# Performance work log

Hardware: AMD Instinct MI355X
Metric: run time of the kernel (lower is better)

## Reference

```python
import jax, jax.numpy as jnp
import numpy as np

T, B, E, H = 2048, 2, 1024, 16
D = E // H

def setup_inputs() -> dict:
    key = jax.random.key(0)
    ks = jax.random.split(key, 5)
    s = 1.0 / np.sqrt(E)  # keep projection weights at sane scale
    return {
        "query": jax.random.normal(ks[0], (T, B, E), jnp.float32),
        "Wq": jax.random.normal(ks[1], (E, E), jnp.float32) * s,
        "bq": jnp.zeros((E,), jnp.float32),
        "Wk": jax.random.normal(ks[2], (E, E), jnp.float32) * s,
        "bk": jnp.zeros((E,), jnp.float32),
        "Wv": jax.random.normal(ks[3], (E, E), jnp.float32) * s,
        "bv": jnp.zeros((E,), jnp.float32),
        "Wo": jax.random.normal(ks[4], (E, E), jnp.float32) * s,
        "bo": jnp.zeros((E,), jnp.float32),
    }

def reference(query, Wq, bq, Wk, bk, Wv, bv, Wo, bo):
    # query: [T, B, E] (fairseq time-first). self-attention path.
    scaling = D ** -0.5
    q = (query @ Wq.T + bq) * scaling          # [T,B,E]
    k = query @ Wk.T + bk                      # [T,B,E]
    v = query @ Wv.T + bv                      # [T,B,E]
    # split heads: [T,B,H,D]
    q = q.reshape(T, B, H, D)
    k = k.reshape(T, B, H, D)
    v = v.reshape(T, B, H, D)
    # attention scores [B,H,T,S]
    scores = jnp.einsum("tbhd,sbhd->bhts", q, k)
    probs = jax.nn.softmax(scores, axis=-1)
    # weighted values -> [T,B,H,D]
    attn = jnp.einsum("bhts,sbhd->tbhd", probs, v).reshape(T, B, E)
    return attn @ Wo.T + bo                    # [T,B,E]
```

## Files before the change

kernel.cpp:

```cpp
#include <hip/hip_runtime.h>
#include <hip/hip_bf16.h>

#define T_DIM 2048

typedef __attribute__((ext_vector_type(8))) short short8_t;
typedef short8_t __attribute__((may_alias)) short8_a;
typedef __attribute__((ext_vector_type(4))) short short4_t;
typedef short4_t __attribute__((may_alias)) short4_a;
typedef __attribute__((ext_vector_type(4))) float f32x4;
typedef __attribute__((ext_vector_type(16))) float f32x16;
typedef __attribute__((ext_vector_type(4))) float float4_t;
typedef float4_t __attribute__((may_alias)) float4_a;
typedef __attribute__((ext_vector_type(4))) unsigned int u32x4;

__device__ __forceinline__ short f2bf(float f) {
    unsigned int u = __builtin_bit_cast(unsigned int, f);
    unsigned int r = (u + 0x7fffu + ((u >> 16) & 1u)) >> 16;
    return (short)r;
}

__device__ __forceinline__ void gl_lds16(const short* g, short* l) {
    __builtin_amdgcn_global_load_lds(
        (const __attribute__((address_space(1))) void*)g,
        (__attribute__((address_space(3))) void*)l, 16, 0, 0);
}

__global__ __launch_bounds__(256) void cvt_kernel(const float* __restrict__ in,
                                                  short* __restrict__ out, int n) {
    int i = (blockIdx.x * 256 + threadIdx.x) * 8;
    if (i >= n) return;
    float4_a a = *(const float4_a*)(in + i);
    float4_a b = *(const float4_a*)(in + i + 4);
    short8_a r;
    r[0] = f2bf(a[0]); r[1] = f2bf(a[1]); r[2] = f2bf(a[2]); r[3] = f2bf(a[3]);
    r[4] = f2bf(b[0]); r[5] = f2bf(b[1]); r[6] = f2bf(b[2]); r[7] = f2bf(b[3]);
    *(short8_a*)(out + i) = r;
}

__global__ __launch_bounds__(256) void cvt_w4(const float* __restrict__ w0, const float* __restrict__ w1,
                                              const float* __restrict__ w2, const float* __restrict__ w3,
                                              short* __restrict__ o0, short* __restrict__ o1,
                                              short* __restrict__ o2, short* __restrict__ o3) {
    const float* in; short* out;
    switch (blockIdx.y) {
        case 0: in = w0; out = o0; break;
        case 1: in = w1; out = o1; break;
        case 2: in = w2; out = o2; break;
        default: in = w3; out = o3; break;
    }
    int i = (blockIdx.x * 256 + threadIdx.x) * 8;
    float4_a a = *(const float4_a*)(in + i);
    float4_a b = *(const float4_a*)(in + i + 4);
    short8_a r;
    r[0] = f2bf(a[0]); r[1] = f2bf(a[1]); r[2] = f2bf(a[2]); r[3] = f2bf(a[3]);
    r[4] = f2bf(b[0]); r[5] = f2bf(b[1]); r[6] = f2bf(b[2]); r[7] = f2bf(b[3]);
    *(short8_a*)(out + i) = r;
}

template <int BM, int BN, int MODE>
__global__ __launch_bounds__(256) void gemm_lds(const short* __restrict__ A,
                                                const short* __restrict__ W,
                                                const float* __restrict__ b0,
                                                const float* __restrict__ b1,
                                                const float* __restrict__ b2,
                                                short* __restrict__ o0,
                                                short* __restrict__ o1,
                                                short* __restrict__ o2,
                                                float* __restrict__ of) {
    constexpr int FM = BM / 32;
    constexpr int FN = BN / 32;
    __shared__ short As[BM * 32];
    __shared__ short Bs[BN * 32];

    const int tid = threadIdx.x;
    const int l = tid & 63, w = tid >> 6;
    const int wm = w >> 1, wn = w & 1;
    const int m0 = blockIdx.y * BM, n0 = blockIdx.x * BN;
    const int l15 = l & 15, l4 = l >> 4;
    const int lr = l >> 2, lc = (l & 3) * 8;

    f32x4 acc[FM][FN];
#pragma unroll
    for (int i = 0; i < FM; i++)
#pragma unroll
        for (int j = 0; j < FN; j++) {
            f32x4 z = {0.f, 0.f, 0.f, 0.f};
            acc[i][j] = z;
        }

    const short* Ab = A + (m0 + lr) * 1024 + lc;
    const short* Wb = W + (n0 + lr) * 1024 + lc;

    for (int k0 = 0; k0 < 1024; k0 += 32) {
#pragma unroll
        for (int j = 0; j < BM / 64; j++) {
            int base = (j * 4 + w) * 16;
            gl_lds16(Ab + base * 1024 + k0, &As[base * 32]);
        }
#pragma unroll
        for (int j = 0; j < BN / 64; j++) {
            int base = (j * 4 + w) * 16;
            gl_lds16(Wb + base * 1024 + k0, &Bs[base * 32]);
        }
        __syncthreads();

        short8_t af[FM], bf[FN];
#pragma unroll
        for (int m = 0; m < FM; m++)
            af[m] = *(const short8_a*)&As[(wm * (BM / 2) + m * 16 + l15) * 32 + l4 * 8];
#pragma unroll
        for (int n = 0; n < FN; n++)
            bf[n] = *(const short8_a*)&Bs[(wn * (BN / 2) + n * 16 + l15) * 32 + l4 * 8];
#pragma unroll
        for (int m = 0; m < FM; m++)
#pragma unroll
            for (int n = 0; n < FN; n++)
                acc[m][n] = __builtin_amdgcn_mfma_f32_16x16x32_bf16(af[m], bf[n], acc[m][n], 0, 0, 0);
        __syncthreads();
    }

    if (MODE == 3) {
#pragma unroll
        for (int n = 0; n < FN; n++) {
            int col = n0 + wn * (BN / 2) + n * 16 + l15;
            float bv = b0[col];
#pragma unroll
            for (int m = 0; m < FM; m++)
#pragma unroll
                for (int i = 0; i < 4; i++) {
                    int row = m0 + wm * (BM / 2) + m * 16 + l4 * 4 + i;
                    of[row * 1024 + col] = acc[m][n][i] + bv;
                }
        }
    } else {
        const int proj = n0 >> 10;
        const float* bias = proj == 0 ? b0 : (proj == 1 ? b1 : b2);
        short* outp = proj == 0 ? o0 : (proj == 1 ? o1 : o2);
#pragma unroll
        for (int n = 0; n < FN; n++) {
            int cw = (n0 + wn * (BN / 2) + n * 16 + l15) & 1023;
            float bv = bias[cw];
            int h = cw >> 6, d = cw & 63;
#pragma unroll
            for (int m = 0; m < FM; m++)
#pragma unroll
                for (int i = 0; i < 4; i++) {
                    int row = m0 + wm * (BM / 2) + m * 16 + l4 * 4 + i;
                    float v = acc[m][n][i] + bv;
                    if (proj == 0) v *= 0.18033688011112042f;
                    int bb = row & 1, t = row >> 1;
                    if (proj == 2)
                        outp[((bb * 16 + h) * 64 + d) * 2048 + t] = f2bf(v);
                    else
                        outp[((bb * 16 + h) * 2048 + t) * 64 + d] = f2bf(v);
                }
        }
    }
}

__device__ __forceinline__ float max16(const f32x16 v) {
    float a0 = fmaxf(fmaxf(v[0], v[1]), v[2]);
    float a1 = fmaxf(fmaxf(v[3], v[4]), v[5]);
    float a2 = fmaxf(fmaxf(v[6], v[7]), v[8]);
    float a3 = fmaxf(fmaxf(v[9], v[10]), v[11]);
    float a4 = fmaxf(fmaxf(v[12], v[13]), v[14]);
    float b0 = fmaxf(fmaxf(a0, a1), v[15]);
    float b1 = fmaxf(fmaxf(a2, a3), a4);
    return fmaxf(b0, b1);
}

__global__ __launch_bounds__(256) void flash_attn(const short* __restrict__ Q,
                                                  const short* __restrict__ K,
                                                  const short* __restrict__ Vt,
                                                  short* __restrict__ O) {
    __shared__ short Ks[2][64 * 64];
    __shared__ short Vs[2][64 * 64];

    const int tid = threadIdx.x, l = tid & 63, w = tid >> 6;
    const int l31 = l & 31, hi = l >> 5;
    const int e = l31 & 7;
    const int bh = blockIdx.y;
    const int b = bh >> 4, hh = bh & 15;
    const int qrow = blockIdx.x * 128 + w * 32 + l31;

    const short* Qp = Q + bh * (T_DIM * 64);
    const short* Kp = K + bh * (T_DIM * 64);
    const short* Vp = Vt + bh * (64 * T_DIM);

    short8_t qf[4];
#pragma unroll
    for (int c = 0; c < 4; c++)
        qf[c] = *(const short8_a*)&Qp[qrow * 64 + c * 16 + hi * 8];

    f32x16 oacc[2];
    f32x16 lacc;
#pragma unroll
    for (int i = 0; i < 16; i++) { oacc[0][i] = 0.f; oacc[1][i] = 0.f; lacc[i] = 0.f; }
    float mrow = -1e30f;

    short8_t ones;
#pragma unroll
    for (int j = 0; j < 8; j++) ones[j] = (short)0x3F80;

    const int srow0 = tid >> 3, sch = tid & 7;
    const int srow1 = srow0 + 32;
    const int kslot0 = (sch ^ (srow0 & 7)) * 8;
    const int kslot1 = (sch ^ (srow1 & 7)) * 8;

    short8_t kpre[2], vpre[2];
    kpre[0] = *(const short8_a*)&Kp[srow0 * 64 + sch * 8];
    kpre[1] = *(const short8_a*)&Kp[srow1 * 64 + sch * 8];
    vpre[0] = *(const short8_a*)&Vp[srow0 * 2048 + sch * 8];
    vpre[1] = *(const short8_a*)&Vp[srow1 * 2048 + sch * 8];
    *(short8_a*)&Ks[0][srow0 * 64 + kslot0] = kpre[0];
    *(short8_a*)&Ks[0][srow1 * 64 + kslot1] = kpre[1];
    *(short8_a*)&Vs[0][srow0 * 64 + kslot0] = vpre[0];
    *(short8_a*)&Vs[0][srow1 * 64 + kslot1] = vpre[1];

    auto body = [&](const short* kc, const short* vc, short* kn, short* vn, int it) {
        __syncthreads();
        if (it + 1 < 32) {
            int s0 = (it + 1) * 64;
            kpre[0] = *(const short8_a*)&Kp[(s0 + srow0) * 64 + sch * 8];
            kpre[1] = *(const short8_a*)&Kp[(s0 + srow1) * 64 + sch * 8];
            vpre[0] = *(const short8_a*)&Vp[srow0 * 2048 + s0 + sch * 8];
            vpre[1] = *(const short8_a*)&Vp[srow1 * 2048 + s0 + sch * 8];
        }

        f32x16 st[2];
#pragma unroll
        for (int r = 0; r < 2; r++) {
#pragma unroll
            for (int i = 0; i < 16; i++) st[r][i] = 0.f;
#pragma unroll
            for (int c = 0; c < 4; c++) {
                short8_t kf = *(const short8_a*)&kc[(r * 32 + l31) * 64 + ((2 * c + hi) ^ e) * 8];
                st[r] = __builtin_amdgcn_mfma_f32_32x32x16_bf16(kf, qf[c], st[r], 0, 0, 0);
            }
        }

        float pmax = fmaxf(max16(st[0]), max16(st[1]));
        pmax = fmaxf(pmax, __shfl_xor(pmax, 32));
        if (__any(pmax > mrow + 8.f)) {
            float mn = fmaxf(mrow, pmax);
            float sc = exp2f(mrow - mn);
            mrow = mn;
            lacc[0] *= sc;
#pragma unroll
            for (int dd = 0; dd < 2; dd++)
#pragma unroll
                for (int i = 0; i < 16; i++) oacc[dd][i] *= sc;
        }
#pragma unroll
        for (int r = 0; r < 2; r++)
#pragma unroll
            for (int i = 0; i < 16; i++) st[r][i] = exp2f(st[r][i] - mrow);

#pragma unroll
        for (int r = 0; r < 2; r++) {
            unsigned pk8[8];
#pragma unroll
            for (int u = 0; u < 8; u++) {
                unsigned t;
                asm("v_cvt_pk_bf16_f32 %0, %1, %2" : "=v"(t) : "v"(st[r][2 * u]), "v"(st[r][2 * u + 1]));
                pk8[u] = t;
            }
#pragma unroll
            for (int cc = 0; cc < 2; cc++) {
                unsigned A0 = pk8[4 * cc + 0], B0 = pk8[4 * cc + 2];
                unsigned A1 = pk8[4 * cc + 1], B1 = pk8[4 * cc + 3];
                asm("v_permlane32_swap_b32 %0, %1" : "+v"(A0), "+v"(B0));
                asm("v_permlane32_swap_b32 %0, %1" : "+v"(A1), "+v"(B1));
                u32x4 pu = {A0, A1, B0, B1};
                short8_t pf = __builtin_bit_cast(short8_t, pu);
                lacc = __builtin_amdgcn_mfma_f32_32x32x16_bf16(ones, pf, lacc, 0, 0, 0);
#pragma unroll
                for (int dd = 0; dd < 2; dd++) {
                    short8_t vf = *(const short8_a*)&vc[(dd * 32 + l31) * 64 +
                                                        ((4 * r + 2 * cc + hi) ^ e) * 8];
                    oacc[dd] = __builtin_amdgcn_mfma_f32_32x32x16_bf16(vf, pf, oacc[dd], 0, 0, 0);
                }
            }
        }

        if (it + 1 < 32) {
            *(short8_a*)&kn[srow0 * 64 + kslot0] = kpre[0];
            *(short8_a*)&kn[srow1 * 64 + kslot1] = kpre[1];
            *(short8_a*)&vn[srow0 * 64 + kslot0] = vpre[0];
            *(short8_a*)&vn[srow1 * 64 + kslot1] = vpre[1];
        }
    };

    for (int it = 0; it < 32; it += 2) {
        body(Ks[0], Vs[0], Ks[1], Vs[1], it);
        body(Ks[1], Vs[1], Ks[0], Vs[0], it + 1);
    }

    float rl = 1.0f / lacc[0];
#pragma unroll
    for (int dd = 0; dd < 2; dd++)
#pragma unroll
        for (int g = 0; g < 4; g++) {
            short4_t o4;
#pragma unroll
            for (int i = 0; i < 4; i++) o4[i] = f2bf(oacc[dd][4 * g + i] * rl);
            *(short4_a*)&O[(qrow * 2 + b) * 1024 + hh * 64 + dd * 32 + g * 8 + hi * 4] = o4;
        }
}

extern "C" void kernel_launch(void* const* d_in, const int* in_sizes, int n_in,
                              void* d_out, int out_size, void* d_ws, size_t ws_size,
                              hipStream_t stream) {
    const float* query = (const float*)d_in[0];
    const float* Wq = (const float*)d_in[1];
    const float* bq = (const float*)d_in[2];
    const float* Wk = (const float*)d_in[3];
    const float* bk = (const float*)d_in[4];
    const float* Wv = (const float*)d_in[5];
    const float* bv = (const float*)d_in[6];
    const float* Wo = (const float*)d_in[7];
    const float* bo = (const float*)d_in[8];

    short* Xbf = (short*)d_ws;
    short* Wqb = Xbf + 4194304;
    short* Wkb = Wqb + 1048576;
    short* Wvb = Wkb + 1048576;
    short* Wob = Wvb + 1048576;
    short* Qb = Wob + 1048576;
    short* Kb = Qb + 4194304;
    short* Vtb = Kb + 4194304;
    short* attnb = Xbf;

    cvt_kernel<<<2048, 256, 0, stream>>>(query, Xbf, 4194304);
    cvt_w4<<<dim3(512, 4), 256, 0, stream>>>(Wq, Wk, Wv, Wo, Wqb, Wkb, Wvb, Wob);

    gemm_lds<128, 128, 4><<<dim3(24, 32), 256, 0, stream>>>(Xbf, Wqb, bq, bk, bv,
                                                            Qb, Kb, Vtb, nullptr);

    flash_attn<<<dim3(16, 32), 256, 0, stream>>>(Qb, Kb, Vtb, attnb);

    gemm_lds<64, 128, 3><<<dim3(8, 64), 256, 0, stream>>>(attnb, Wob, bo, nullptr, nullptr,
                                                          nullptr, nullptr, nullptr, (float*)d_out);
}
```

Baseline: 136.7 us.

## Split attention KV range across two wave groups and merge conversion kernels

The flash attention block grows to 512 threads. Two groups of four waves each process half of the key/value sequence for the same 128 query rows, and their partial softmax states are merged through LDS at the end. The goal is more waves in flight on a grid of only 512 blocks and a shorter serial loop per block. The cost is extra LDS, a final merge step and higher register pressure under launch_bounds(512,4). Separately, the input and weight bf16 conversion kernels are fused into one launch, removing one kernel launch.

```diff
diff --git a/kernel.cpp b/kernel.cpp
--- a/kernel.cpp
+++ b/kernel.cpp
@@ -25,32 +25,25 @@
         (__attribute__((address_space(3))) void*)l, 16, 0, 0);
 }
 
-__global__ __launch_bounds__(256) void cvt_kernel(const float* __restrict__ in,
-                                                  short* __restrict__ out, int n) {
-    int i = (blockIdx.x * 256 + threadIdx.x) * 8;
-    if (i >= n) return;
-    float4_a a = *(const float4_a*)(in + i);
-    float4_a b = *(const float4_a*)(in + i + 4);
-    short8_a r;
-    r[0] = f2bf(a[0]); r[1] = f2bf(a[1]); r[2] = f2bf(a[2]); r[3] = f2bf(a[3]);
-    r[4] = f2bf(b[0]); r[5] = f2bf(b[1]); r[6] = f2bf(b[2]); r[7] = f2bf(b[3]);
-    *(short8_a*)(out + i) = r;
-}
-
-__global__ __launch_bounds__(256) void cvt_w4(const float* __restrict__ w0, const float* __restrict__ w1,
-                                              const float* __restrict__ w2, const float* __restrict__ w3,
-                                              short* __restrict__ o0, short* __restrict__ o1,
-                                              short* __restrict__ o2, short* __restrict__ o3) {
-    const float* in; short* out;
-    switch (blockIdx.y) {
-        case 0: in = w0; out = o0; break;
-        case 1: in = w1; out = o1; break;
-        case 2: in = w2; out = o2; break;
-        default: in = w3; out = o3; break;
-    }
-    int i = (blockIdx.x * 256 + threadIdx.x) * 8;
-    float4_a a = *(const float4_a*)(in + i);
-    float4_a b = *(const float4_a*)(in + i + 4);
+__global__ __launch_bounds__(256) void cvt_all(const float* __restrict__ query,
+                                               const float* __restrict__ Wq,
+                                               const float* __restrict__ Wk,
+                                               const float* __restrict__ Wv,
+                                               const float* __restrict__ Wo,
+                                               short* __restrict__ out) {
+    const int bx = blockIdx.x;
+    const int i = bx * 2048 + threadIdx.x * 8;
+    const float* s;
+    if (bx < 2048) {
+        s = query + i;
+    } else {
+        int j = i - 4194304;
+        int wsel = j >> 20;
+        const float* wp = wsel == 0 ? Wq : (wsel == 1 ? Wk : (wsel == 2 ? Wv : Wo));
+        s = wp + (j & 1048575);
+    }
+    float4_a a = *(const float4_a*)s;
+    float4_a b = *(const float4_a*)(s + 4);
     short8_a r;
     r[0] = f2bf(a[0]); r[1] = f2bf(a[1]); r[2] = f2bf(a[2]); r[3] = f2bf(a[3]);
     r[4] = f2bf(b[0]); r[5] = f2bf(b[1]); r[6] = f2bf(b[2]); r[7] = f2bf(b[3]);
@@ -169,23 +162,24 @@
     return fmaxf(b0, b1);
 }
 
-__global__ __launch_bounds__(256) void flash_attn(const short* __restrict__ Q,
-                                                  const short* __restrict__ K,
-                                                  const short* __restrict__ Vt,
-                                                  short* __restrict__ O) {
-    __shared__ short Ks[2][64 * 64];
-    __shared__ short Vs[2][64 * 64];
+__global__ __launch_bounds__(512, 4) void flash_attn(const short* __restrict__ Q,
+                                                     const short* __restrict__ K,
+                                                     const short* __restrict__ Vt,
+                                                     short* __restrict__ O) {
+    __shared__ short Ks[2][2][64 * 64];
+    __shared__ short Vs[2][2][64 * 64];
 
     const int tid = threadIdx.x, l = tid & 63, w = tid >> 6;
+    const int g = w >> 2, w4 = w & 3;
     const int l31 = l & 31, hi = l >> 5;
     const int e = l31 & 7;
     const int bh = blockIdx.y;
     const int b = bh >> 4, hh = bh & 15;
-    const int qrow = blockIdx.x * 128 + w * 32 + l31;
+    const int qrow = blockIdx.x * 128 + w4 * 32 + l31;
 
     const short* Qp = Q + bh * (T_DIM * 64);
-    const short* Kp = K + bh * (T_DIM * 64);
-    const short* Vp = Vt + bh * (64 * T_DIM);
+    const short* Kp = K + bh * (T_DIM * 64) + g * 1024 * 64;
+    const short* Vp = Vt + bh * (64 * T_DIM) + g * 1024;
 
     short8_t qf[4];
 #pragma unroll
@@ -202,7 +196,8 @@
 #pragma unroll
     for (int j = 0; j < 8; j++) ones[j] = (short)0x3F80;
 
-    const int srow0 = tid >> 3, sch = tid & 7;
+    const int tidg = tid & 255;
+    const int srow0 = tidg >> 3, sch = tidg & 7;
     const int srow1 = srow0 + 32;
     const int kslot0 = (sch ^ (srow0 & 7)) * 8;
     const int kslot1 = (sch ^ (srow1 & 7)) * 8;
@@ -212,14 +207,14 @@
     kpre[1] = *(const short8_a*)&Kp[srow1 * 64 + sch * 8];
     vpre[0] = *(const short8_a*)&Vp[srow0 * 2048 + sch * 8];
     vpre[1] = *(const short8_a*)&Vp[srow1 * 2048 + sch * 8];
-    *(short8_a*)&Ks[0][srow0 * 64 + kslot0] = kpre[0];
-    *(short8_a*)&Ks[0][srow1 * 64 + kslot1] = kpre[1];
-    *(short8_a*)&Vs[0][srow0 * 64 + kslot0] = vpre[0];
-    *(short8_a*)&Vs[0][srow1 * 64 + kslot1] = vpre[1];
+    *(short8_a*)&Ks[g][0][srow0 * 64 + kslot0] = kpre[0];
+    *(short8_a*)&Ks[g][0][srow1 * 64 + kslot1] = kpre[1];
+    *(short8_a*)&Vs[g][0][srow0 * 64 + kslot0] = vpre[0];
+    *(short8_a*)&Vs[g][0][srow1 * 64 + kslot1] = vpre[1];
 
     auto body = [&](const short* kc, const short* vc, short* kn, short* vn, int it) {
         __syncthreads();
-        if (it + 1 < 32) {
+        if (it + 1 < 16) {
             int s0 = (it + 1) * 64;
             kpre[0] = *(const short8_a*)&Kp[(s0 + srow0) * 64 + sch * 8];
             kpre[1] = *(const short8_a*)&Kp[(s0 + srow1) * 64 + sch * 8];
@@ -283,7 +278,7 @@
             }
         }
 
-        if (it + 1 < 32) {
+        if (it + 1 < 16) {
             *(short8_a*)&kn[srow0 * 64 + kslot0] = kpre[0];
             *(short8_a*)&kn[srow1 * 64 + kslot1] = kpre[1];
             *(short8_a*)&vn[srow0 * 64 + kslot0] = vpre[0];
@@ -291,21 +286,45 @@
         }
     };
 
-    for (int it = 0; it < 32; it += 2) {
-        body(Ks[0], Vs[0], Ks[1], Vs[1], it);
-        body(Ks[1], Vs[1], Ks[0], Vs[0], it + 1);
-    }
-
-    float rl = 1.0f / lacc[0];
-#pragma unroll
-    for (int dd = 0; dd < 2; dd++)
-#pragma unroll
-        for (int g = 0; g < 4; g++) {
-            short4_t o4;
-#pragma unroll
-            for (int i = 0; i < 4; i++) o4[i] = f2bf(oacc[dd][4 * g + i] * rl);
-            *(short4_a*)&O[(qrow * 2 + b) * 1024 + hh * 64 + dd * 32 + g * 8 + hi * 4] = o4;
-        }
+    for (int it = 0; it < 16; it += 2) {
+        body(Ks[g][0], Vs[g][0], Ks[g][1], Vs[g][1], it);
+        body(Ks[g][1], Vs[g][1], Ks[g][0], Vs[g][0], it + 1);
+    }
+
+    __syncthreads();
+    float* xo = (float*)&Ks[0][0][0];
+    float* xml = (float*)&Vs[0][0][0];
+    if (g == 1) {
+#pragma unroll
+        for (int dd = 0; dd < 2; dd++)
+#pragma unroll
+            for (int g4 = 0; g4 < 4; g4++) {
+                f32x4 v = {oacc[dd][4 * g4], oacc[dd][4 * g4 + 1],
+                           oacc[dd][4 * g4 + 2], oacc[dd][4 * g4 + 3]};
+                *(float4_a*)&xo[w4 * 2048 + (dd * 4 + g4) * 256 + l * 4] = v;
+            }
+        xml[w4 * 128 + l] = mrow;
+        xml[w4 * 128 + 64 + l] = lacc[0];
+    }
+    __syncthreads();
+    if (g == 0) {
+        float m1 = xml[w4 * 128 + l];
+        float l1 = xml[w4 * 128 + 64 + l];
+        float mm = fmaxf(mrow, m1);
+        float s0 = exp2f(mrow - mm), s1 = exp2f(m1 - mm);
+        float rl = 1.0f / (lacc[0] * s0 + l1 * s1);
+#pragma unroll
+        for (int dd = 0; dd < 2; dd++)
+#pragma unroll
+            for (int g4 = 0; g4 < 4; g4++) {
+                f32x4 o1 = *(const float4_a*)&xo[w4 * 2048 + (dd * 4 + g4) * 256 + l * 4];
+                short4_t o4;
+#pragma unroll
+                for (int i = 0; i < 4; i++)
+                    o4[i] = f2bf((oacc[dd][4 * g4 + i] * s0 + o1[i] * s1) * rl);
+                *(short4_a*)&O[(qrow * 2 + b) * 1024 + hh * 64 + dd * 32 + g4 * 8 + hi * 4] = o4;
+            }
+    }
 }
 
 extern "C" void kernel_launch(void* const* d_in, const int* in_sizes, int n_in,
@@ -331,13 +350,12 @@
     short* Vtb = Kb + 4194304;
     short* attnb = Xbf;
 
-    cvt_kernel<<<2048, 256, 0, stream>>>(query, Xbf, 4194304);
-    cvt_w4<<<dim3(512, 4), 256, 0, stream>>>(Wq, Wk, Wv, Wo, Wqb, Wkb, Wvb, Wob);
+    cvt_all<<<4096, 256, 0, stream>>>(query, Wq, Wk, Wv, Wo, Xbf);
 
     gemm_lds<128, 128, 4><<<dim3(24, 32), 256, 0, stream>>>(Xbf, Wqb, bq, bk, bv,
                                                             Qb, Kb, Vtb, nullptr);
 
-    flash_attn<<<dim3(16, 32), 256, 0, stream>>>(Qb, Kb, Vtb, attnb);
+    flash_attn<<<dim3(16, 32), 512, 0, stream>>>(Qb, Kb, Vtb, attnb);
 
     gemm_lds<64, 128, 3><<<dim3(8, 64), 256, 0, stream>>>(attnb, Wob, bo, nullptr, nullptr,
                                                           nullptr, nullptr, nullptr, (float*)d_out);
```

New measurement: 183.4 us. 34.1% more time.

## Stage flash-attention K/V via direct global-to-LDS loads, swizzle blocks, merge converts

Applied to the files above, without the earlier changes.

The flash-attention kernel now double-buffers K and V tiles with global_load_lds, which writes global memory straight into LDS in the same XOR-swizzled layout. This replaces the old path that prefetched into registers and then stored to LDS at the end of each iteration. It also remaps block IDs so that neighbouring workgroups spread across heads and query tiles. The two fp32-to-bf16 conversion kernels are merged into one launch over a contiguous workspace. The intent is to cut register pressure and VGPR-to-LDS store traffic and to save one launch, but correctness now depends on the loads into LDS being complete before each barrier.

```diff
diff --git a/kernel.cpp b/kernel.cpp
--- a/kernel.cpp
+++ b/kernel.cpp
@@ -25,32 +25,25 @@
         (__attribute__((address_space(3))) void*)l, 16, 0, 0);
 }
 
-__global__ __launch_bounds__(256) void cvt_kernel(const float* __restrict__ in,
-                                                  short* __restrict__ out, int n) {
-    int i = (blockIdx.x * 256 + threadIdx.x) * 8;
-    if (i >= n) return;
-    float4_a a = *(const float4_a*)(in + i);
-    float4_a b = *(const float4_a*)(in + i + 4);
-    short8_a r;
-    r[0] = f2bf(a[0]); r[1] = f2bf(a[1]); r[2] = f2bf(a[2]); r[3] = f2bf(a[3]);
-    r[4] = f2bf(b[0]); r[5] = f2bf(b[1]); r[6] = f2bf(b[2]); r[7] = f2bf(b[3]);
-    *(short8_a*)(out + i) = r;
-}
-
-__global__ __launch_bounds__(256) void cvt_w4(const float* __restrict__ w0, const float* __restrict__ w1,
-                                              const float* __restrict__ w2, const float* __restrict__ w3,
-                                              short* __restrict__ o0, short* __restrict__ o1,
-                                              short* __restrict__ o2, short* __restrict__ o3) {
-    const float* in; short* out;
-    switch (blockIdx.y) {
-        case 0: in = w0; out = o0; break;
-        case 1: in = w1; out = o1; break;
-        case 2: in = w2; out = o2; break;
-        default: in = w3; out = o3; break;
+__global__ __launch_bounds__(256) void cvt_all(const float* __restrict__ query,
+                                               const float* __restrict__ Wq,
+                                               const float* __restrict__ Wk,
+                                               const float* __restrict__ Wv,
+                                               const float* __restrict__ Wo,
+                                               short* __restrict__ out) {
+    const int bx = blockIdx.x;
+    const int i = bx * 2048 + threadIdx.x * 8;
+    const float* s;
+    if (bx < 2048) {
+        s = query + i;
+    } else {
+        int j = i - 4194304;
+        int wsel = j >> 20;
+        const float* wp = wsel == 0 ? Wq : (wsel == 1 ? Wk : (wsel == 2 ? Wv : Wo));
+        s = wp + (j & 1048575);
     }
-    int i = (blockIdx.x * 256 + threadIdx.x) * 8;
-    float4_a a = *(const float4_a*)(in + i);
-    float4_a b = *(const float4_a*)(in + i + 4);
+    float4_a a = *(const float4_a*)s;
+    float4_a b = *(const float4_a*)(s + 4);
     short8_a r;
     r[0] = f2bf(a[0]); r[1] = f2bf(a[1]); r[2] = f2bf(a[2]); r[3] = f2bf(a[3]);
     r[4] = f2bf(b[0]); r[5] = f2bf(b[1]); r[6] = f2bf(b[2]); r[7] = f2bf(b[3]);
@@ -179,9 +172,13 @@
     const int tid = threadIdx.x, l = tid & 63, w = tid >> 6;
     const int l31 = l & 31, hi = l >> 5;
     const int e = l31 & 7;
-    const int bh = blockIdx.y;
+
+    const int bid = blockIdx.x + (blockIdx.y << 4);
+    const int swz = (bid & 7) * 64 + (bid >> 3);
+    const int qt = swz & 15, bh = swz >> 4;
+
     const int b = bh >> 4, hh = bh & 15;
-    const int qrow = blockIdx.x * 128 + w * 32 + l31;
+    const int qrow = qt * 128 + w * 32 + l31;
 
     const short* Qp = Q + bh * (T_DIM * 64);
     const short* Kp = K + bh * (T_DIM * 64);
@@ -202,30 +199,32 @@
 #pragma unroll
     for (int j = 0; j < 8; j++) ones[j] = (short)0x3F80;
 
-    const int srow0 = tid >> 3, sch = tid & 7;
-    const int srow1 = srow0 + 32;
-    const int kslot0 = (sch ^ (srow0 & 7)) * 8;
-    const int kslot1 = (sch ^ (srow1 & 7)) * 8;
-
-    short8_t kpre[2], vpre[2];
-    kpre[0] = *(const short8_a*)&Kp[srow0 * 64 + sch * 8];
-    kpre[1] = *(const short8_a*)&Kp[srow1 * 64 + sch * 8];
-    vpre[0] = *(const short8_a*)&Vp[srow0 * 2048 + sch * 8];
-    vpre[1] = *(const short8_a*)&Vp[srow1 * 2048 + sch * 8];
-    *(short8_a*)&Ks[0][srow0 * 64 + kslot0] = kpre[0];
-    *(short8_a*)&Ks[0][srow1 * 64 + kslot1] = kpre[1];
-    *(short8_a*)&Vs[0][srow0 * 64 + kslot0] = vpre[0];
-    *(short8_a*)&Vs[0][srow1 * 64 + kslot1] = vpre[1];
-
-    auto body = [&](const short* kc, const short* vc, short* kn, short* vn, int it) {
+    const int lrow = l >> 3;
+    const int lch = (l & 7) ^ (lrow & 7);
+    const int j0 = 2 * w, j1 = 2 * w + 1;
+    const short* kg0 = Kp + (j0 * 8 + lrow) * 64 + lch * 8;
+    const short* kg1 = Kp + (j1 * 8 + lrow) * 64 + lch * 8;
+    const short* vg0 = Vp + (j0 * 8 + lrow) * 2048 + lch * 8;
+    const short* vg1 = Vp + (j1 * 8 + lrow) * 2048 + lch * 8;
+
+    auto stage = [&](int it, int buf) {
+        const int koff = it * 4096;
+        const int voff = it * 64;
+        gl_lds16(kg0 + koff, &Ks[buf][j0 * 512]);
+        gl_lds16(kg1 + koff, &Ks[buf][j1 * 512]);
+        gl_lds16(vg0 + voff, &Vs[buf][j0 * 512]);
+        gl_lds16(vg1 + voff, &Vs[buf][j1 * 512]);
+    };
+
+    stage(0, 0);
+
+    for (int it = 0; it < 32; ++it) {
+        const int cur = it & 1;
         __syncthreads();
-        if (it + 1 < 32) {
-            int s0 = (it + 1) * 64;
-            kpre[0] = *(const short8_a*)&Kp[(s0 + srow0) * 64 + sch * 8];
-            kpre[1] = *(const short8_a*)&Kp[(s0 + srow1) * 64 + sch * 8];
-            vpre[0] = *(const short8_a*)&Vp[srow0 * 2048 + s0 + sch * 8];
-            vpre[1] = *(const short8_a*)&Vp[srow1 * 2048 + s0 + sch * 8];
-        }
+        if (it + 1 < 32) stage(it + 1, cur ^ 1);
+
+        const short* kc = Ks[cur];
+        const short* vc = Vs[cur];
 
         f32x16 st[2];
 #pragma unroll
@@ -282,18 +281,6 @@
                 }
             }
         }
-
-        if (it + 1 < 32) {
-            *(short8_a*)&kn[srow0 * 64 + kslot0] = kpre[0];
-            *(short8_a*)&kn[srow1 * 64 + kslot1] = kpre[1];
-            *(short8_a*)&vn[srow0 * 64 + kslot0] = vpre[0];
-            *(short8_a*)&vn[srow1 * 64 + kslot1] = vpre[1];
-        }
-    };
-
-    for (int it = 0; it < 32; it += 2) {
-        body(Ks[0], Vs[0], Ks[1], Vs[1], it);
-        body(Ks[1], Vs[1], Ks[0], Vs[0], it + 1);
     }
 
     float rl = 1.0f / lacc[0];
@@ -331,8 +318,7 @@
     short* Vtb = Kb + 4194304;
     short* attnb = Xbf;
 
-    cvt_kernel<<<2048, 256, 0, stream>>>(query, Xbf, 4194304);
-    cvt_w4<<<dim3(512, 4), 256, 0, stream>>>(Wq, Wk, Wv, Wo, Wqb, Wkb, Wvb, Wob);
+    cvt_all<<<4096, 256, 0, stream>>>(query, Wq, Wk, Wv, Wo, Xbf);
 
     gemm_lds<128, 128, 4><<<dim3(24, 32), 256, 0, stream>>>(Xbf, Wqb, bq, bk, bv,
                                                             Qb, Kb, Vtb, nullptr);
```

After: 142.1 us. 1.04x slower.
